# Kernel tuning notes

Hardware: AMD Instinct MI355X
Metric: run time of the kernel (lower is better)

Reference implementation:

```python
import jax, jax.numpy as jnp
import numpy as np

jax.config.update("jax_enable_x64", True)

# Dims (see shape_source): batch, heads, q-len, kv-len, head-channels, quant group
B, H, T, S, HC = 2, 16, 1024, 1024, 128
G = 8            # group_size from A/R_QUANT_PARAMS
SCALE_SHIFT = 14 # combined dequant shift applied to integer QK scores before softmax
O_SM = 14        # fixed-point offset of the integer softmax output (LUT-style)
PROB_QMAX = 255.0  # 8-bit unsigned probability mantissa (R_QUANT_PARAMS n_bits=8)


def _dequant_po2(q, s):
    """q: int mantissas [..., N], s: nonneg po2 shift exponents [..., N//G].
    Emulates (q << s) per group of G channels (pot_scale activation quantizer)."""
    s_full = jnp.repeat(s, G, axis=-1)
    return q.astype(jnp.float64) * jnp.exp2(s_full.astype(jnp.float64))


def setup_inputs() -> dict:
    key = jax.random.key(0)
    ks = jax.random.split(key, 6)
    # signed 8-bit mantissas in [-128, 127]
    q_q = jax.random.randint(ks[0], (B, H, T, HC), 0, 256, dtype=jnp.int32) - 128
    k_q = jax.random.randint(ks[1], (B, H, S, HC), 0, 256, dtype=jnp.int32) - 128
    vt_q = jax.random.randint(ks[2], (B, H, HC, S), 0, 256, dtype=jnp.int32) - 128
    # nonnegative power-of-two shifts, one per group of G=8
    q_s = jax.random.randint(ks[3], (B, H, T, HC // G), 0, 4, dtype=jnp.int32)
    k_s = jax.random.randint(ks[4], (B, H, S, HC // G), 0, 4, dtype=jnp.int32)
    vt_s = jax.random.randint(ks[5], (B, H, HC, S // G), 0, 4, dtype=jnp.int32)
    return {"q_q": q_q, "q_s": q_s, "k_q": k_q, "k_s": k_s, "vt_q": vt_q, "vt_s": vt_s}


def reference(q_q, q_s, k_q, k_s, vt_q, vt_s):
    # ---- shift_qk_matmul: (q_q << q_s) @ (k_q << k_s)^T in float64, truncated to int64
    q = _dequant_po2(q_q, q_s)                       # [B,H,T,HC] f64
    k = _dequant_po2(k_q, k_s)                       # [B,H,S,HC] f64
    scores = jnp.einsum("bhtc,bhsc->bhts", q, k).astype(jnp.int64)

    # ---- integer softmax emulation: rescale integer scores, softmax, then
    # re-quantize probabilities with an 8-bit per-group (G=8 along S) po2 scale
    logits = scores.astype(jnp.float32) * np.float32(2.0 ** (-SCALE_SHIFT) / np.sqrt(HC))
    p = jax.nn.softmax(logits, axis=-1)              # [B,H,T,S]
    val = jnp.round(p * (2.0 ** O_SM))               # fixed-point probs (ints)
    vg = val.reshape(B, H, T, S // G, G)
    gmax = jnp.max(vg, axis=-1, keepdims=True)
    r_shift = jnp.clip(jnp.ceil(jnp.log2(jnp.maximum(gmax, 1.0) / PROB_QMAX)), 0.0, None)
    r_q = jnp.clip(jnp.round(vg / jnp.exp2(r_shift)), 0.0, PROB_QMAX)
    r = (r_q * jnp.exp2(r_shift)).reshape(B, H, T, S).astype(jnp.float64)  # (r_q << r_s)

    # ---- shift_rv_matmul: r @ (vt_q << vt_s)^T in float64, truncated to int64
    vt = _dequant_po2(vt_q, vt_s)                    # [B,H,HC,S] f64
    a = jnp.einsum("bhts,bhcs->bhtc", r, vt).astype(jnp.int64)  # [B,H,T,HC]
    return a
```

## Files before the change

### kernel.cpp

```cpp
#include <hip/hip_runtime.h>
#include <string.h>


typedef int   v4i __attribute__((ext_vector_type(4)));
typedef float v4f __attribute__((ext_vector_type(4)));
typedef short v8s __attribute__((ext_vector_type(8)));

#define BHN 32
#define TN  1024
#define SN  1024
#define HCN 128
#define TT  16
#define RST 1032
#define KD_BH 262144
#define VD_BH 262144
#define WS_NEED ((size_t)BHN*(KD_BH+VD_BH))

__device__ __forceinline__ unsigned pack_b(int b0,int b1,int b2,int b3){
    return (unsigned)((b0&255)|((b1&255)<<8)|((b2&255)<<16)|((b3&255)<<24));
}

__device__ __forceinline__ void dig16(const int* __restrict__ p, int s0, int s1,
                                      v4i& hi, v4i& lo){
    #pragma unroll
    for (int wi=0; wi<4; ++wi){
        v4i m = *(const v4i*)(p + wi*4);
        int s = (wi<2) ? s0 : s1;
        int d0=m[0]<<s, d1=m[1]<<s, d2=m[2]<<s, d3=m[3]<<s;
        hi[wi] = (int)pack_b(d0>>4,d1>>4,d2>>4,d3>>4);
        lo[wi] = (int)pack_b(d0&15,d1&15,d2&15,d3&15);
    }
}

__device__ __forceinline__ unsigned short bf16_of_int(int v){
    return (unsigned short)(__float_as_uint((float)v) >> 16);
}

__global__ __launch_bounds__(256) void digitize(
    const int* __restrict__ k_q, const int* __restrict__ k_s,
    const int* __restrict__ vt_q, const int* __restrict__ vt_s,
    unsigned char* __restrict__ kd, unsigned char* __restrict__ vd)
{
    const int g = blockIdx.x*256 + threadIdx.x;
    const int ioff = g*16;
    if (blockIdx.y == 0){
        int row = ioff>>7, c0 = ioff&127;
        int s0 = k_s[(row<<4)+(c0>>3)], s1 = k_s[(row<<4)+(c0>>3)+1];
        v4i hi, lo;
        dig16(k_q + ioff, s0, s1, hi, lo);
        int bh = row>>10, srow = row&1023;
        int ch = srow>>7, lr = srow&127, n = lr>>4, l15 = lr&15;
        int kc = c0>>6, q4 = (c0>>4)&3;
        size_t base = (size_t)bh*KD_BH + (size_t)ch*32768u
                    + (size_t)(n*4096 + kc*2048 + (q4*16+l15)*16);
        *(v4i*)(kd + base)        = hi;
        *(v4i*)(kd + base + 1024) = lo;
    } else {
        int grow = ioff>>10, s4 = ioff&1023;
        int sc0 = vt_s[(grow<<7)+(s4>>3)], sc1 = vt_s[(grow<<7)+(s4>>3)+1];
        int bh = grow>>7, chan = grow&127;
        int n = chan>>4, l15 = chan&15;
        int kb = s4>>5, q0 = (s4>>3)&3;
        const int* vp = vt_q + ioff;
        #pragma unroll
        for (int h=0; h<2; ++h){
            int s = (h==0) ? sc0 : sc1;
            unsigned wds[4];
            #pragma unroll
            for (int j=0; j<4; ++j){
                int a = vp[h*8 + j*2]   << s;
                int b = vp[h*8 + j*2+1] << s;
                wds[j] = (unsigned)bf16_of_int(a) | ((unsigned)bf16_of_int(b) << 16);
            }
            size_t base = (size_t)bh*VD_BH
                        + (size_t)(((kb*8 + n)*64 + (q0+h)*16 + l15)*16);
            *(v4i*)(vd + base) = v4i{(int)wds[0],(int)wds[1],(int)wds[2],(int)wds[3]};
        }
    }
}

template<bool PK>
__global__ __launch_bounds__(256,4) void mha_mfma(
    const int* __restrict__ q_q, const int* __restrict__ q_s,
    const int* __restrict__ k_q, const int* __restrict__ k_s,
    const int* __restrict__ vt_q, const int* __restrict__ vt_s,
    const unsigned char* __restrict__ kd, const unsigned char* __restrict__ vd,
    int* __restrict__ out)
{
    __shared__ unsigned short rbuf[16*RST];
    __shared__ float red[128];

    const int tid  = threadIdx.x;
    const int ln   = tid & 15;
    const int qd4  = (tid >> 4) & 3;
    const int w    = tid >> 6;
    const int lane = tid & 63;
    const int blk = blockIdx.x;
    const int bh  = ((blk>>9)<<3) | (blk&7);
    const int t0  = ((blk>>3)&63) * TT;

    v4i qfh[2], qfl[2];
    {
        const int* qrow  = q_q + (size_t)(bh*TN + t0 + ln)*HCN;
        const int* qsrow = q_s + (size_t)(bh*TN + t0 + ln)*16;
        #pragma unroll
        for (int kc=0; kc<2; ++kc){
            int gi = kc*8 + qd4*2;
            dig16(qrow + kc*64 + qd4*16, qsrow[gi], qsrow[gi+1], qfh[kc], qfl[kc]);
        }
    }

    int scv[16][4];

    const v4i* kb_ = (const v4i*)(kd + (size_t)bh*KD_BH);
    for (int ch=0; ch<8; ++ch){
        #pragma unroll
        for (int i=0;i<2;i++){
            const int n = w*2 + i;
            v4i a2{0,0,0,0}, a1{0,0,0,0}, a0{0,0,0,0};
            #pragma unroll
            for (int kc=0;kc<2;kc++){
                v4i bhv, blv;
                if (PK){
                    const v4i* tb = kb_ + (ch*8+n)*256 + kc*128 + lane;
                    bhv = tb[0];
                    blv = tb[64];
                } else {
                    int srow = bh*SN + ch*128 + n*16 + ln;
                    int cc   = kc*64 + qd4*16;
                    dig16(k_q + (size_t)srow*128 + cc,
                          k_s[srow*16 + (cc>>3)], k_s[srow*16 + (cc>>3) + 1], bhv, blv);
                }
                a2 = __builtin_amdgcn_mfma_i32_16x16x64_i8(qfh[kc], bhv, a2, 0,0,0);
                a1 = __builtin_amdgcn_mfma_i32_16x16x64_i8(qfl[kc], bhv, a1, 0,0,0);
                a1 = __builtin_amdgcn_mfma_i32_16x16x64_i8(qfh[kc], blv, a1, 0,0,0);
                a0 = __builtin_amdgcn_mfma_i32_16x16x64_i8(qfl[kc], blv, a0, 0,0,0);
            }
            int st = ch*2 + i;
            #pragma unroll
            for (int r=0;r<4;r++)
                scv[st][r] = (a2[r]<<8) + (a1[r]<<4) + a0[r];
        }
    }

    const float CS = (float)(6.103515625e-05 / 11.313708498984760390566);
    float mx[4], sm[4];
    #pragma unroll
    for (int r=0;r<4;r++){
        float m_ = -3.0e38f;
        #pragma unroll
        for (int st=0;st<16;st++) m_ = fmaxf(m_, (float)scv[st][r]*CS);
        #pragma unroll
        for (int o=8;o>0;o>>=1) m_ = fmaxf(m_, __shfl_xor(m_, o));
        mx[r] = m_;
    }
    if (ln == 0){
        #pragma unroll
        for (int r=0;r<4;r++) red[w*16 + qd4*4 + r] = mx[r];
    }
    __syncthreads();
    #pragma unroll
    for (int r=0;r<4;r++){
        float m_ = fmaxf(fmaxf(red[qd4*4+r], red[16+qd4*4+r]),
                         fmaxf(red[32+qd4*4+r], red[48+qd4*4+r]));
        float s_ = 0.f;
        #pragma unroll
        for (int st=0;st<16;st++){
            float e = expf((float)scv[st][r]*CS - m_);
            scv[st][r] = __float_as_int(e);
            s_ += e;
        }
        #pragma unroll
        for (int o=8;o>0;o>>=1) s_ += __shfl_xor(s_, o);
        sm[r] = s_;
    }
    if (ln == 0){
        #pragma unroll
        for (int r=0;r<4;r++) red[64 + w*16 + qd4*4 + r] = sm[r];
    }
    __syncthreads();
    float inv14[4];
    #pragma unroll
    for (int r=0;r<4;r++){
        float s_ = red[64+qd4*4+r] + red[80+qd4*4+r] + red[96+qd4*4+r] + red[112+qd4*4+r];
        inv14[r] = 16384.0f / s_;
    }

    #pragma unroll
    for (int st=0;st<16;st++){
        int colb = (st>>1)*128 + (w*2+(st&1))*16;
        #pragma unroll
        for (int r=0;r<4;r++){
            float val = rintf(__int_as_float(scv[st][r]) * inv14[r]);
            float g = val;
            g = fmaxf(g, __shfl_xor(g, 1));
            g = fmaxf(g, __shfl_xor(g, 2));
            g = fmaxf(g, __shfl_xor(g, 4));
            int gi = max((int)g, 1);
            int x = gi - 1;
            int e = 31 - __clz(x | 255);
            int sh = (e - 7) + ((x >> (e - 7)) == 255);
            float rq = fminf(rintf(val * __int_as_float((127-sh)<<23)), 255.0f);
            int rv = ((int)rq) << sh;
            int row = qd4*4 + r;
            int col = colb + ln;
            int gs  = (col>>3) ^ (row&7);
            rbuf[row*RST + gs*8 + (col&7)] = bf16_of_int(rv);
        }
    }
    __syncthreads();

    const v4i* vb = (const v4i*)(vd + (size_t)bh*VD_BH);
    v4f acc0{0,0,0,0}, acc1{0,0,0,0};
    #pragma unroll 4
    for (int kb=0; kb<32; ++kb){
        v8s af = *(const v8s*)(rbuf + ln*RST + (((kb*4+qd4) ^ (ln&7))<<3));
        v4i b0, b1;
        if (PK){
            b0 = vb[(kb*8 + w*2    )*64 + lane];
            b1 = vb[(kb*8 + w*2 + 1)*64 + lane];
        } else {
            #pragma unroll
            for (int i=0;i<2;i++){
                int chan = (w*2+i)*16 + ln;
                const int* vp = vt_q + (size_t)(bh*HCN + chan)*SN + kb*32 + qd4*8;
                int s = vt_s[(bh*HCN + chan)*128 + kb*4 + qd4];
                unsigned wd[4];
                #pragma unroll
                for (int j=0;j<4;j++){
                    int a = vp[j*2]   << s;
                    int b = vp[j*2+1] << s;
                    wd[j] = (unsigned)bf16_of_int(a) | ((unsigned)bf16_of_int(b)<<16);
                }
                v4i t{(int)wd[0],(int)wd[1],(int)wd[2],(int)wd[3]};
                if (i==0) b0 = t; else b1 = t;
            }
        }
        v8s bs0, bs1;
        memcpy(&bs0, &b0, 16);
        memcpy(&bs1, &b1, 16);
        acc0 = __builtin_amdgcn_mfma_f32_16x16x32_bf16(af, bs0, acc0, 0,0,0);
        acc1 = __builtin_amdgcn_mfma_f32_16x16x32_bf16(af, bs1, acc1, 0,0,0);
    }
    #pragma unroll
    for (int r=0;r<4;r++){
        size_t o = (size_t)(bh*TN + t0 + qd4*4 + r)*HCN + (w*2)*16 + ln;
        out[o]      = (int)rintf(acc0[r]);
        out[o + 16] = (int)rintf(acc1[r]);
    }
}

extern "C" void kernel_launch(void* const* d_in, const int* in_sizes, int n_in,
                              void* d_out, int out_size, void* d_ws, size_t ws_size,
                              hipStream_t stream) {
    const int* q_q  = (const int*)d_in[0];
    const int* q_s  = (const int*)d_in[1];
    const int* k_q  = (const int*)d_in[2];
    const int* k_s  = (const int*)d_in[3];
    const int* vt_q = (const int*)d_in[4];
    const int* vt_s = (const int*)d_in[5];
    int* out = (int*)d_out;

    unsigned char* kd = (unsigned char*)d_ws;
    unsigned char* vd = kd + (size_t)BHN*KD_BH;

    if (ws_size >= WS_NEED){
        digitize<<<dim3(1024,2), 256, 0, stream>>>(k_q,k_s,vt_q,vt_s, kd,vd);
        mha_mfma<true><<<dim3(2048), 256, 0, stream>>>(
            q_q,q_s,k_q,k_s,vt_q,vt_s, kd,vd, out);
    } else {
        mha_mfma<false><<<dim3(2048), 256, 0, stream>>>(
            q_q,q_s,k_q,k_s,vt_q,vt_s, kd,vd, out);
    }
}
```

Before: 172.5 us.

## Coalesce digitize writes, use native exp2, move group requantization to LDS pass

The digitize kernel is remapped so each wave writes one contiguous packed tile, giving coalesced 16-byte stores for both K and V preprocessing. Softmax now pre-multiplies scores by log2(e) and computes the exponential with the raw v_exp_f32 instruction instead of expf, which may change rounding slightly. Per-group probability requantization moves out of the register loop with its three cross-lane shuffles. It now runs as a separate pass that reads 8-value groups from shared memory as vectors. That pass costs an extra barrier and an extra LDS read/write round trip.

```diff
diff --git a/kernel.cpp b/kernel.cpp
--- a/kernel.cpp
+++ b/kernel.cpp
@@ -41,41 +41,36 @@
     const int* __restrict__ vt_q, const int* __restrict__ vt_s,
     unsigned char* __restrict__ kd, unsigned char* __restrict__ vd)
 {
-    const int g = blockIdx.x*256 + threadIdx.x;
-    const int ioff = g*16;
-    if (blockIdx.y == 0){
-        int row = ioff>>7, c0 = ioff&127;
-        int s0 = k_s[(row<<4)+(c0>>3)], s1 = k_s[(row<<4)+(c0>>3)+1];
+    const int w    = threadIdx.x >> 6;
+    const int lane = threadIdx.x & 63;
+    const int l15  = lane & 15;
+    const int task = blockIdx.x*4 + w;
+    if (task < 4096){
+        const int kc = task & 1, n = (task>>1)&7, ch = (task>>4)&7, bh = task>>7;
+        const int q4   = lane >> 4;
+        const int srow = bh*SN + ch*128 + n*16 + l15;
+        const int gb   = srow*16 + kc*8 + q4*2;
         v4i hi, lo;
-        dig16(k_q + ioff, s0, s1, hi, lo);
-        int bh = row>>10, srow = row&1023;
-        int ch = srow>>7, lr = srow&127, n = lr>>4, l15 = lr&15;
-        int kc = c0>>6, q4 = (c0>>4)&3;
-        size_t base = (size_t)bh*KD_BH + (size_t)ch*32768u
-                    + (size_t)(n*4096 + kc*2048 + (q4*16+l15)*16);
+        dig16(k_q + (size_t)srow*HCN + kc*64 + q4*16, k_s[gb], k_s[gb+1], hi, lo);
+        size_t base = (size_t)bh*KD_BH + (size_t)(ch*32768 + n*4096 + kc*2048 + lane*16);
         *(v4i*)(kd + base)        = hi;
         *(v4i*)(kd + base + 1024) = lo;
     } else {
-        int grow = ioff>>10, s4 = ioff&1023;
-        int sc0 = vt_s[(grow<<7)+(s4>>3)], sc1 = vt_s[(grow<<7)+(s4>>3)+1];
-        int bh = grow>>7, chan = grow&127;
-        int n = chan>>4, l15 = chan&15;
-        int kb = s4>>5, q0 = (s4>>3)&3;
-        const int* vp = vt_q + ioff;
-        #pragma unroll
-        for (int h=0; h<2; ++h){
-            int s = (h==0) ? sc0 : sc1;
-            unsigned wds[4];
-            #pragma unroll
-            for (int j=0; j<4; ++j){
-                int a = vp[h*8 + j*2]   << s;
-                int b = vp[h*8 + j*2+1] << s;
-                wds[j] = (unsigned)bf16_of_int(a) | ((unsigned)bf16_of_int(b) << 16);
-            }
-            size_t base = (size_t)bh*VD_BH
-                        + (size_t)(((kb*8 + n)*64 + (q0+h)*16 + l15)*16);
-            *(v4i*)(vd + base) = v4i{(int)wds[0],(int)wds[1],(int)wds[2],(int)wds[3]};
-        }
+        const int t  = task - 4096;
+        const int n  = t & 7, kb = (t>>3)&31, bh = t>>8;
+        const int sub = lane >> 4;
+        const int row = bh*HCN + n*16 + l15;
+        const int* vp = vt_q + (size_t)row*SN + kb*32 + sub*8;
+        const int s   = vt_s[row*128 + kb*4 + sub];
+        unsigned wds[4];
+        #pragma unroll
+        for (int j=0;j<4;j++){
+            int a = vp[j*2]   << s;
+            int b = vp[j*2+1] << s;
+            wds[j] = (unsigned)bf16_of_int(a) | ((unsigned)bf16_of_int(b) << 16);
+        }
+        size_t base = (size_t)bh*VD_BH + (size_t)(((kb*8 + n)*64 + lane)*16);
+        *(v4i*)(vd + base) = v4i{(int)wds[0],(int)wds[1],(int)wds[2],(int)wds[3]};
     }
 }
 
@@ -87,7 +82,7 @@
     const unsigned char* __restrict__ kd, const unsigned char* __restrict__ vd,
     int* __restrict__ out)
 {
-    __shared__ unsigned short rbuf[16*RST];
+    __shared__ __align__(16) unsigned short rbuf[16*RST];
     __shared__ float red[128];
 
     const int tid  = threadIdx.x;
@@ -143,13 +138,18 @@
         }
     }
 
-    const float CS = (float)(6.103515625e-05 / 11.313708498984760390566);
-    float mx[4], sm[4];
+    const float CS2 = (float)(6.103515625e-05 / 11.313708498984760390566
+                              * 1.4426950408889634074);
+    float mx[4];
     #pragma unroll
     for (int r=0;r<4;r++){
         float m_ = -3.0e38f;
         #pragma unroll
-        for (int st=0;st<16;st++) m_ = fmaxf(m_, (float)scv[st][r]*CS);
+        for (int st=0;st<16;st++){
+            float f = (float)scv[st][r] * CS2;
+            scv[st][r] = __float_as_int(f);
+            m_ = fmaxf(m_, f);
+        }
         #pragma unroll
         for (int o=8;o>0;o>>=1) m_ = fmaxf(m_, __shfl_xor(m_, o));
         mx[r] = m_;
@@ -159,6 +159,7 @@
         for (int r=0;r<4;r++) red[w*16 + qd4*4 + r] = mx[r];
     }
     __syncthreads();
+    float sm[4];
     #pragma unroll
     for (int r=0;r<4;r++){
         float m_ = fmaxf(fmaxf(red[qd4*4+r], red[16+qd4*4+r]),
@@ -166,7 +167,9 @@
         float s_ = 0.f;
         #pragma unroll
         for (int st=0;st<16;st++){
-            float e = expf((float)scv[st][r]*CS - m_);
+            float t = __int_as_float(scv[st][r]) - m_;
+            float e;
+            asm("v_exp_f32 %0, %1" : "=v"(e) : "v"(t));
             scv[st][r] = __float_as_int(e);
             s_ += e;
         }
@@ -191,21 +194,39 @@
         int colb = (st>>1)*128 + (w*2+(st&1))*16;
         #pragma unroll
         for (int r=0;r<4;r++){
-            float val = rintf(__int_as_float(scv[st][r]) * inv14[r]);
-            float g = val;
-            g = fmaxf(g, __shfl_xor(g, 1));
-            g = fmaxf(g, __shfl_xor(g, 2));
-            g = fmaxf(g, __shfl_xor(g, 4));
-            int gi = max((int)g, 1);
-            int x = gi - 1;
-            int e = 31 - __clz(x | 255);
-            int sh = (e - 7) + ((x >> (e - 7)) == 255);
-            float rq = fminf(rintf(val * __int_as_float((127-sh)<<23)), 255.0f);
-            int rv = ((int)rq) << sh;
+            int val = (int)rintf(__int_as_float(scv[st][r]) * inv14[r]);
             int row = qd4*4 + r;
             int col = colb + ln;
             int gs  = (col>>3) ^ (row&7);
-            rbuf[row*RST + gs*8 + (col&7)] = bf16_of_int(rv);
+            rbuf[row*RST + gs*8 + (col&7)] = (unsigned short)val;
+        }
+    }
+    __syncthreads();
+
+    {
+        const int prow = tid >> 4;
+        const int pc   = tid & 15;
+        unsigned short* rp = rbuf + prow*RST;
+        #pragma unroll
+        for (int i=0;i<8;i++){
+            const int cg  = pc + 16*i;
+            const int off = (cg ^ (prow & 7)) << 3;
+            v8s v = *(const v8s*)(rp + off);
+            int g01 = max((int)v[0], (int)v[1]), g23 = max((int)v[2], (int)v[3]);
+            int g45 = max((int)v[4], (int)v[5]), g67 = max((int)v[6], (int)v[7]);
+            int gmax = max(max(g01, g23), max(g45, g67));
+            int gi = max(gmax, 1);
+            int x  = gi - 1;
+            int e2 = 31 - __clz(x | 255);
+            int sh = (e2 - 7) + ((x >> (e2 - 7)) == 255);
+            float isc = __int_as_float((127 - sh) << 23);
+            v8s o;
+            #pragma unroll
+            for (int j=0;j<8;j++){
+                float rq = fminf(rintf((float)(int)v[j] * isc), 255.0f);
+                o[j] = (short)bf16_of_int(((int)rq) << sh);
+            }
+            *(v8s*)(rp + off) = o;
         }
     }
     __syncthreads();
@@ -265,7 +286,7 @@
     unsigned char* vd = kd + (size_t)BHN*KD_BH;
 
     if (ws_size >= WS_NEED){
-        digitize<<<dim3(1024,2), 256, 0, stream>>>(k_q,k_s,vt_q,vt_s, kd,vd);
+        digitize<<<dim3(3072), 256, 0, stream>>>(k_q,k_s,vt_q,vt_s, kd,vd);
         mha_mfma<true><<<dim3(2048), 256, 0, stream>>>(
             q_q,q_s,k_q,k_s,vt_q,vt_s, kd,vd, out);
     } else {
```

After: 156.4 us. -9.3%, faster.
